# Optimization experiments

Hardware: AMD Instinct MI355X
Metric: run time of the kernel (lower is better)

The kernel has to match this reference:

```python
import jax, jax.numpy as jnp
import numpy as np

DIM = 768
HEADS = 12
HEAD_DIM = DIM // HEADS
B, N = 4, 2048


def setup_inputs() -> dict:
    key = jax.random.key(0)
    ks = jax.random.split(key, 5)
    s = 0.02
    return {
        "x": jax.random.normal(ks[0], (B, N, DIM), dtype=jnp.float32),
        "w_qkv": jax.random.normal(ks[1], (DIM, 3 * DIM), dtype=jnp.float32) * s,
        "b_qkv": jnp.zeros((3 * DIM,), dtype=jnp.float32),
        "w_proj": jax.random.normal(ks[2], (DIM, DIM), dtype=jnp.float32) * s,
        "b_proj": jnp.zeros((DIM,), dtype=jnp.float32),
    }


def reference(x, w_qkv, b_qkv, w_proj, b_proj):
    b, n, c = x.shape
    scale = HEAD_DIM ** -0.5
    qkv = x @ w_qkv + b_qkv                       # [B,N,3C]
    qkv = qkv.reshape(b, n, 3, HEADS, HEAD_DIM)
    q = qkv[:, :, 0].transpose(0, 2, 1, 3)        # [B,H,N,D]
    k = qkv[:, :, 1].transpose(0, 2, 1, 3)
    v = qkv[:, :, 2].transpose(0, 2, 1, 3)
    attn = jnp.einsum("bhqd,bhkd->bhqk", q, k) * scale
    attn = jax.nn.softmax(attn, axis=-1)
    out = jnp.einsum("bhqk,bhkd->bhqd", attn, v)  # [B,H,N,D]
    out = out.transpose(0, 2, 1, 3).reshape(b, n, c)
    return out @ w_proj + b_proj
```

## Files before the change

### kernel.cpp

```cpp
#include <hip/hip_runtime.h>

typedef short sh8 __attribute__((ext_vector_type(8)));
typedef short sh4 __attribute__((ext_vector_type(4)));
typedef float f32x4 __attribute__((ext_vector_type(4)));
typedef float f32x16 __attribute__((ext_vector_type(16)));
typedef unsigned u32x4 __attribute__((ext_vector_type(4)));

extern "C" __device__ float __ocml_native_exp2_f32(float);

__device__ __forceinline__ short f2bf(float f) {
  unsigned u = __builtin_bit_cast(unsigned, f);
  u += 0x7fffu + ((u >> 16) & 1u);
  return (short)(u >> 16);
}

__device__ __forceinline__ void gload16(const short* g, short* l) {
  __builtin_amdgcn_global_load_lds(
      (const __attribute__((address_space(1))) unsigned*)g,
      (__attribute__((address_space(3))) unsigned*)l, 16, 0, 0);
}

__global__ void cast_f32_bf16(const float* __restrict__ in, short* __restrict__ out, int n) {
  int i = (blockIdx.x * blockDim.x + threadIdx.x) * 4;
  if (i >= n) return;
  float4 f = *(const float4*)(in + i);
  sh4 o;
  o.x = f2bf(f.x); o.y = f2bf(f.y); o.z = f2bf(f.z); o.w = f2bf(f.w);
  *(sh4*)(out + i) = o;
}

__global__ void transpose_cast(const float* __restrict__ in, short* __restrict__ out, int K, int Nn) {
  int idx = blockIdx.x * blockDim.x + threadIdx.x;
  if (idx >= K * Nn) return;
  int k = idx / Nn;
  int n = idx - k * Nn;
  out[(size_t)n * K + k] = f2bf(in[idx]);
}

template <int OUTF32>
__global__ __launch_bounds__(256) void gemm_bt(
    const short* __restrict__ A, const short* __restrict__ Bt,
    const float* __restrict__ bias, void* __restrict__ Cv,
    int M, int Nn, int K) {
  __shared__ short As[2][128][32];
  __shared__ short Bs[2][128][32];
  const int t = threadIdx.x;
  const int wave = t >> 6, lane = t & 63, quad = lane >> 4, l15 = lane & 15;
  const int wm = (wave >> 1) * 64, wn = (wave & 1) * 64;
  const int row0 = blockIdx.y * 128, col0 = blockIdx.x * 128;
  f32x4 acc[4][4] = {};

  const int srow = t >> 2;
  const int ssl = ((t & 3) ^ ((t >> 3) & 3)) * 8;
  const short* Asrc0 = A + (size_t)(row0 + srow) * K + ssl;
  const short* Asrc1 = A + (size_t)(row0 + 64 + srow) * K + ssl;
  const short* Bsrc0 = Bt + (size_t)(col0 + srow) * K + ssl;
  const short* Bsrc1 = Bt + (size_t)(col0 + 64 + srow) * K + ssl;
  short* AsF = &As[0][0][0];
  short* BsF = &Bs[0][0][0];
  const int wdst = wave * 512;

  const int soA = (quad ^ ((l15 >> 1) & 3)) * 8;

  gload16(Asrc0, AsF + wdst);
  gload16(Asrc1, AsF + 2048 + wdst);
  gload16(Bsrc0, BsF + wdst);
  gload16(Bsrc1, BsF + 2048 + wdst);
  __syncthreads();

  int cur = 0;
  for (int k0 = 0; k0 < K; k0 += 32) {
    if (k0 + 32 < K) {
      short* Ad = AsF + (cur ^ 1) * 4096 + wdst;
      short* Bd = BsF + (cur ^ 1) * 4096 + wdst;
      gload16(Asrc0 + k0 + 32, Ad);
      gload16(Asrc1 + k0 + 32, Ad + 2048);
      gload16(Bsrc0 + k0 + 32, Bd);
      gload16(Bsrc1 + k0 + 32, Bd + 2048);
    }
    const short* Ab = AsF + cur * 4096;
    const short* Bb = BsF + cur * 4096;
    sh8 af[4], bfv[4];
#pragma unroll
    for (int i = 0; i < 4; i++) af[i] = *(const sh8*)&Ab[(wm + i * 16 + l15) * 32 + soA];
#pragma unroll
    for (int j = 0; j < 4; j++) bfv[j] = *(const sh8*)&Bb[(wn + j * 16 + l15) * 32 + soA];
#pragma unroll
    for (int i = 0; i < 4; i++)
#pragma unroll
      for (int j = 0; j < 4; j++)
        acc[i][j] = __builtin_amdgcn_mfma_f32_16x16x32_bf16(af[i], bfv[j], acc[i][j], 0, 0, 0);
    __syncthreads();
    cur ^= 1;
  }

#pragma unroll
  for (int i = 0; i < 4; i++)
#pragma unroll
    for (int j = 0; j < 4; j++) {
      int r = row0 + wm + i * 16 + quad * 4;
      int c = col0 + wn + j * 16 + l15;
      float bv = bias[c];
#pragma unroll
      for (int e = 0; e < 4; e++) {
        float v = acc[i][j][e] + bv;
        if (OUTF32)
          ((float*)Cv)[(size_t)(r + e) * Nn + c] = v;
        else
          ((short*)Cv)[(size_t)(r + e) * Nn + c] = f2bf(v);
      }
    }
}

__global__ __launch_bounds__(256) void gemm_qkv(
    const short* __restrict__ A, const short* __restrict__ Bt,
    const float* __restrict__ bias,
    short* __restrict__ Qh, short* __restrict__ Kh, short* __restrict__ Vh) {
  const int K = 768;
  __shared__ short As[2][128][32];
  __shared__ short Bs[2][128][32];
  const int t = threadIdx.x;
  const int wave = t >> 6, lane = t & 63, quad = lane >> 4, l15 = lane & 15;
  const int wm = (wave >> 1) * 64, wn = (wave & 1) * 64;
  const int row0 = blockIdx.y * 128, col0 = blockIdx.x * 128;
  f32x4 acc[4][4] = {};

  const int srow = t >> 2;
  const int ssl = ((t & 3) ^ ((t >> 3) & 3)) * 8;
  const short* Asrc0 = A + (size_t)(row0 + srow) * K + ssl;
  const short* Asrc1 = A + (size_t)(row0 + 64 + srow) * K + ssl;
  const short* Bsrc0 = Bt + (size_t)(col0 + srow) * K + ssl;
  const short* Bsrc1 = Bt + (size_t)(col0 + 64 + srow) * K + ssl;
  short* AsF = &As[0][0][0];
  short* BsF = &Bs[0][0][0];
  const int wdst = wave * 512;

  const int soA = (quad ^ ((l15 >> 1) & 3)) * 8;

  gload16(Asrc0, AsF + wdst);
  gload16(Asrc1, AsF + 2048 + wdst);
  gload16(Bsrc0, BsF + wdst);
  gload16(Bsrc1, BsF + 2048 + wdst);
  __syncthreads();

  int cur = 0;
  for (int k0 = 0; k0 < K; k0 += 32) {
    if (k0 + 32 < K) {
      short* Ad = AsF + (cur ^ 1) * 4096 + wdst;
      short* Bd = BsF + (cur ^ 1) * 4096 + wdst;
      gload16(Asrc0 + k0 + 32, Ad);
      gload16(Asrc1 + k0 + 32, Ad + 2048);
      gload16(Bsrc0 + k0 + 32, Bd);
      gload16(Bsrc1 + k0 + 32, Bd + 2048);
    }
    const short* Ab = AsF + cur * 4096;
    const short* Bb = BsF + cur * 4096;
    sh8 af[4], bfv[4];
#pragma unroll
    for (int i = 0; i < 4; i++) af[i] = *(const sh8*)&Ab[(wm + i * 16 + l15) * 32 + soA];
#pragma unroll
    for (int j = 0; j < 4; j++) bfv[j] = *(const sh8*)&Bb[(wn + j * 16 + l15) * 32 + soA];
#pragma unroll
    for (int i = 0; i < 4; i++)
#pragma unroll
      for (int j = 0; j < 4; j++)
        acc[i][j] = __builtin_amdgcn_mfma_f32_16x16x32_bf16(af[i], bfv[j], acc[i][j], 0, 0, 0);
    __syncthreads();
    cur ^= 1;
  }

  const int s = col0 >= 1536 ? 2 : (col0 >= 768 ? 1 : 0);
  short* dst = s == 0 ? Qh : (s == 1 ? Kh : Vh);
  const float scl = (s == 0) ? 0.18033688011112042f : 1.0f;

#pragma unroll
  for (int j = 0; j < 4; j++) {
    int c = col0 + wn + j * 16 + l15;
    int hd = c - s * 768;
    int h = hd >> 6;
    float bv = bias[c];
#pragma unroll
    for (int i = 0; i < 4; i++) {
      int rbase = row0 + wm + i * 16 + quad * 4;
#pragma unroll
      for (int e = 0; e < 4; e++) {
        int r = rbase + e;
        int b = r >> 11, n = r & 2047;
        float v = (acc[i][j][e] + bv) * scl;
        dst[(size_t)(b * 12 + h) * 131072 + n * 64 + (hd & 63)] = f2bf(v);
      }
    }
  }
}

__global__ __launch_bounds__(256) void transpose_v(const short* __restrict__ Vh,
                                                   short* __restrict__ VhT) {
  __shared__ short Tl[64][72];
  const int bid = blockIdx.x;
  const int bh = bid >> 5, nt = bid & 31;
  const size_t hb = (size_t)bh * 131072;
  const int t = threadIdx.x;
  const int r0 = t >> 3;
  const int c0 = (t & 7) * 8;
  sh8 a = *(const sh8*)&Vh[hb + (size_t)(nt * 64 + r0) * 64 + c0];
  sh8 b = *(const sh8*)&Vh[hb + (size_t)(nt * 64 + r0 + 32) * 64 + c0];
#pragma unroll
  for (int j = 0; j < 8; j++) Tl[c0 + j][r0] = a[j];
#pragma unroll
  for (int j = 0; j < 8; j++) Tl[c0 + j][r0 + 32] = b[j];
  __syncthreads();
  uint4 w0 = *(const uint4*)&Tl[r0][c0];
  uint4 w1 = *(const uint4*)&Tl[r0 + 32][c0];
  *(uint4*)&VhT[hb + (size_t)r0 * 2048 + nt * 64 + c0] = w0;
  *(uint4*)&VhT[hb + (size_t)(r0 + 32) * 2048 + nt * 64 + c0] = w1;
}

__global__ __launch_bounds__(256, 3) void attn6(const short* __restrict__ Qh,
                                                const short* __restrict__ Kh,
                                                const short* __restrict__ VhT,
                                                short* __restrict__ outb) {
  const int bid = blockIdx.x;
  const int qb = bid / 48;
  const int bh = bid - qb * 48;
  const int t = threadIdx.x;
  const int w = t >> 6, lane = t & 63;
  const int l31 = lane & 31, hi = lane >> 5;

  __shared__ short Kl[2][64][64];
  __shared__ short Vt[2][64][64];

  const size_t hb = (size_t)bh * 131072;

  sh8 qa[4];
  {
    const short* qp = Qh + hb + (size_t)(qb * 128 + w * 32 + l31) * 64 + hi * 8;
    qa[0] = *(const sh8*)(qp);
    qa[1] = *(const sh8*)(qp + 16);
    qa[2] = *(const sh8*)(qp + 32);
    qa[3] = *(const sh8*)(qp + 48);
  }

  f32x16 o[2] = {};
  f32x4 lsv = {};

  const int srow = t >> 3;
  const int ssl = ((t & 7) ^ (srow & 7)) * 8;
  const short* Ksrc = Kh + hb + (size_t)srow * 64 + ssl;
  const short* Vsrc = VhT + hb + (size_t)srow * 2048 + ssl;
  short* KlF = &Kl[0][0][0];
  short* VtF = &Vt[0][0][0];
  const int wdst = w * 512;

  const int sw7 = l31 & 7;
  int rsl[4];
#pragma unroll
  for (int ks = 0; ks < 4; ks++) rsl[ks] = (((ks << 1) | hi) ^ sw7) * 8;

  gload16(Ksrc, KlF + wdst);
  gload16(Ksrc + (size_t)32 * 64, KlF + 2048 + wdst);
  gload16(Vsrc, VtF + wdst);
  gload16(Vsrc + (size_t)32 * 2048, VtF + 2048 + wdst);
  __syncthreads();

  int cur = 0;
  for (int kt = 0; kt < 32; kt++) {
    if (kt < 31) {
      const int key0 = (kt + 1) * 64;
      short* Kd = KlF + (cur ^ 1) * 4096 + wdst;
      short* Vd = VtF + (cur ^ 1) * 4096 + wdst;
      gload16(Ksrc + (size_t)key0 * 64, Kd);
      gload16(Ksrc + (size_t)(key0 + 32) * 64, Kd + 2048);
      gload16(Vsrc + key0, Vd);
      gload16(Vsrc + (size_t)32 * 2048 + key0, Vd + 2048);
    }

    const short* Kb = KlF + cur * 4096;
    const short* Vb = VtF + cur * 4096;

    sh8 pa[4];
#pragma unroll
    for (int kb = 0; kb < 2; kb++) {
      const short* kr = Kb + (kb * 32 + l31) * 64;
      f32x16 s = {};
#pragma unroll
      for (int ks = 0; ks < 4; ks++)
        s = __builtin_amdgcn_mfma_f32_32x32x16_bf16(*(const sh8*)(kr + rsl[ks]), qa[ks], s, 0, 0, 0);
      unsigned u[8];
#pragma unroll
      for (int m = 0; m < 8; m++) {
        float e0 = __ocml_native_exp2_f32(s[2 * m]);
        float e1 = __ocml_native_exp2_f32(s[2 * m + 1]);
        lsv[m & 3] += e0 + e1;
        asm("v_cvt_pk_bf16_f32 %0, %1, %2" : "=v"(u[m]) : "v"(e0), "v"(e1));
      }
      unsigned y0 = (unsigned)__shfl_xor((int)(hi ? u[0] : u[2]), 32, 64);
      unsigned y1 = (unsigned)__shfl_xor((int)(hi ? u[1] : u[3]), 32, 64);
      unsigned y2 = (unsigned)__shfl_xor((int)(hi ? u[4] : u[6]), 32, 64);
      unsigned y3 = (unsigned)__shfl_xor((int)(hi ? u[5] : u[7]), 32, 64);
      unsigned w0 = hi ? y0 : u[0];
      unsigned w1 = hi ? y1 : u[1];
      unsigned w2 = hi ? u[2] : y0;
      unsigned w3 = hi ? u[3] : y1;
      unsigned w4 = hi ? y2 : u[4];
      unsigned w5 = hi ? y3 : u[5];
      unsigned w6 = hi ? u[6] : y2;
      unsigned w7 = hi ? u[7] : y3;
      u32x4 A0 = {w0, w1, w2, w3};
      u32x4 A1 = {w4, w5, w6, w7};
      pa[2 * kb] = __builtin_bit_cast(sh8, A0);
      pa[2 * kb + 1] = __builtin_bit_cast(sh8, A1);
    }

    __builtin_amdgcn_s_setprio(1);
#pragma unroll
    for (int db = 0; db < 2; db++) {
      const short* vr = Vb + (db * 32 + l31) * 64;
#pragma unroll
      for (int ks = 0; ks < 4; ks++)
        o[db] = __builtin_amdgcn_mfma_f32_32x32x16_bf16(pa[ks], *(const sh8*)(vr + rsl[ks]), o[db], 0, 0, 0);
    }
    __builtin_amdgcn_s_setprio(0);
    __syncthreads();
    cur ^= 1;
  }

  float ls = lsv[0] + lsv[1] + lsv[2] + lsv[3];
  ls += __shfl_xor(ls, 32, 64);
  float inv = 1.f / ls;

  const int b = bh / 12, hh = bh - b * 12;
#pragma unroll
  for (int r = 0; r < 16; r++) {
    int qr = (r & 3) + 8 * (r >> 2) + 4 * hi;
    float iv = __shfl(inv, qr, 64);
    int n = qb * 128 + w * 32 + qr;
    short* op = outb + (size_t)(b * 2048 + n) * 768 + hh * 64 + l31;
    op[0] = f2bf(o[0][r] * iv);
    op[32] = f2bf(o[1][r] * iv);
  }
}

extern "C" void kernel_launch(void* const* d_in, const int* in_sizes, int n_in,
                              void* d_out, int out_size, void* d_ws, size_t ws_size,
                              hipStream_t stream) {
  const float* x = (const float*)d_in[0];
  const float* w_qkv = (const float*)d_in[1];
  const float* b_qkv = (const float*)d_in[2];
  const float* w_proj = (const float*)d_in[3];
  const float* b_proj = (const float*)d_in[4];
  float* out = (float*)d_out;

  char* p = (char*)d_ws;
  short* xb = (short*)p;     p += (size_t)8192 * 768 * 2;
  short* wqkvT = (short*)p;  p += (size_t)2304 * 768 * 2;
  short* wprojT = (short*)p; p += (size_t)768 * 768 * 2;
  short* Qh = (short*)p;     p += (size_t)48 * 131072 * 2;
  short* Kh = (short*)p;     p += (size_t)48 * 131072 * 2;
  short* Vh = (short*)p;     p += (size_t)48 * 131072 * 2;
  short* attnb = (short*)p;  p += (size_t)8192 * 768 * 2;
  short* VhT = xb;

  cast_f32_bf16<<<(8192 * 768 / 4) / 256, 256, 0, stream>>>(x, xb, 8192 * 768);
  transpose_cast<<<(768 * 2304 + 255) / 256, 256, 0, stream>>>(w_qkv, wqkvT, 768, 2304);
  transpose_cast<<<(768 * 768 + 255) / 256, 256, 0, stream>>>(w_proj, wprojT, 768, 768);

  dim3 g1(2304 / 128, 8192 / 128);
  gemm_qkv<<<g1, 256, 0, stream>>>(xb, wqkvT, b_qkv, Qh, Kh, Vh);

  transpose_v<<<48 * 32, 256, 0, stream>>>(Vh, VhT);

  attn6<<<16 * 48, 256, 0, stream>>>(Qh, Kh, VhT, attnb);

  dim3 g2(768 / 128, 8192 / 128);
  gemm_bt<1><<<g2, 256, 0, stream>>>(attnb, wprojT, b_proj, out, 8192, 768, 768);
}
```

Before: 248.8 us.

## Triple-buffer LDS tiles with prefetch distance two and partial vmcnt waits

```diff
diff --git a/kernel.cpp b/kernel.cpp
--- a/kernel.cpp
+++ b/kernel.cpp
@@ -18,6 +18,17 @@
   __builtin_amdgcn_global_load_lds(
       (const __attribute__((address_space(1))) unsigned*)g,
       (__attribute__((address_space(3))) unsigned*)l, 16, 0, 0);
+}
+
+__device__ __forceinline__ void wait4_barrier() {
+  asm volatile("s_waitcnt vmcnt(4)" ::: "memory");
+  __builtin_amdgcn_s_barrier();
+  asm volatile("" ::: "memory");
+}
+__device__ __forceinline__ void wait0_barrier() {
+  asm volatile("s_waitcnt vmcnt(0)" ::: "memory");
+  __builtin_amdgcn_s_barrier();
+  asm volatile("" ::: "memory");
 }
 
 __global__ void cast_f32_bf16(const float* __restrict__ in, short* __restrict__ out, int n) {
@@ -42,8 +53,8 @@
     const short* __restrict__ A, const short* __restrict__ Bt,
     const float* __restrict__ bias, void* __restrict__ Cv,
     int M, int Nn, int K) {
-  __shared__ short As[2][128][32];
-  __shared__ short Bs[2][128][32];
+  __shared__ short As[3][128][32];
+  __shared__ short Bs[3][128][32];
   const int t = threadIdx.x;
   const int wave = t >> 6, lane = t & 63, quad = lane >> 4, l15 = lane & 15;
   const int wm = (wave >> 1) * 64, wn = (wave & 1) * 64;
@@ -62,24 +73,32 @@
 
   const int soA = (quad ^ ((l15 >> 1) & 3)) * 8;
 
-  gload16(Asrc0, AsF + wdst);
-  gload16(Asrc1, AsF + 2048 + wdst);
-  gload16(Bsrc0, BsF + wdst);
-  gload16(Bsrc1, BsF + 2048 + wdst);
-  __syncthreads();
-
-  int cur = 0;
-  for (int k0 = 0; k0 < K; k0 += 32) {
-    if (k0 + 32 < K) {
-      short* Ad = AsF + (cur ^ 1) * 4096 + wdst;
-      short* Bd = BsF + (cur ^ 1) * 4096 + wdst;
-      gload16(Asrc0 + k0 + 32, Ad);
-      gload16(Asrc1 + k0 + 32, Ad + 2048);
-      gload16(Bsrc0 + k0 + 32, Bd);
-      gload16(Bsrc1 + k0 + 32, Bd + 2048);
-    }
-    const short* Ab = AsF + cur * 4096;
-    const short* Bb = BsF + cur * 4096;
+  const int T = K >> 5;
+#pragma unroll
+  for (int pt = 0; pt < 2; pt++) {
+    short* Ad = AsF + pt * 4096 + wdst;
+    short* Bd = BsF + pt * 4096 + wdst;
+    const int k0 = pt * 32;
+    gload16(Asrc0 + k0, Ad);
+    gload16(Asrc1 + k0, Ad + 2048);
+    gload16(Bsrc0 + k0, Bd);
+    gload16(Bsrc1 + k0, Bd + 2048);
+  }
+
+  int rb = 0, wb = 2;
+  for (int tt = 0; tt < T; tt++) {
+    if (tt + 1 < T) wait4_barrier(); else wait0_barrier();
+    if (tt + 2 < T) {
+      const int k0 = (tt + 2) * 32;
+      short* Ad = AsF + wb * 4096 + wdst;
+      short* Bd = BsF + wb * 4096 + wdst;
+      gload16(Asrc0 + k0, Ad);
+      gload16(Asrc1 + k0, Ad + 2048);
+      gload16(Bsrc0 + k0, Bd);
+      gload16(Bsrc1 + k0, Bd + 2048);
+    }
+    const short* Ab = AsF + rb * 4096;
+    const short* Bb = BsF + rb * 4096;
     sh8 af[4], bfv[4];
 #pragma unroll
     for (int i = 0; i < 4; i++) af[i] = *(const sh8*)&Ab[(wm + i * 16 + l15) * 32 + soA];
@@ -90,8 +109,8 @@
 #pragma unroll
       for (int j = 0; j < 4; j++)
         acc[i][j] = __builtin_amdgcn_mfma_f32_16x16x32_bf16(af[i], bfv[j], acc[i][j], 0, 0, 0);
-    __syncthreads();
-    cur ^= 1;
+    rb = rb == 2 ? 0 : rb + 1;
+    wb = wb == 2 ? 0 : wb + 1;
   }
 
 #pragma unroll
@@ -117,8 +136,8 @@
     const float* __restrict__ bias,
     short* __restrict__ Qh, short* __restrict__ Kh, short* __restrict__ Vh) {
   const int K = 768;
-  __shared__ short As[2][128][32];
-  __shared__ short Bs[2][128][32];
+  __shared__ short As[3][128][32];
+  __shared__ short Bs[3][128][32];
   const int t = threadIdx.x;
   const int wave = t >> 6, lane = t & 63, quad = lane >> 4, l15 = lane & 15;
   const int wm = (wave >> 1) * 64, wn = (wave & 1) * 64;
@@ -137,24 +156,32 @@
 
   const int soA = (quad ^ ((l15 >> 1) & 3)) * 8;
 
-  gload16(Asrc0, AsF + wdst);
-  gload16(Asrc1, AsF + 2048 + wdst);
-  gload16(Bsrc0, BsF + wdst);
-  gload16(Bsrc1, BsF + 2048 + wdst);
-  __syncthreads();
-
-  int cur = 0;
-  for (int k0 = 0; k0 < K; k0 += 32) {
-    if (k0 + 32 < K) {
-      short* Ad = AsF + (cur ^ 1) * 4096 + wdst;
-      short* Bd = BsF + (cur ^ 1) * 4096 + wdst;
-      gload16(Asrc0 + k0 + 32, Ad);
-      gload16(Asrc1 + k0 + 32, Ad + 2048);
-      gload16(Bsrc0 + k0 + 32, Bd);
-      gload16(Bsrc1 + k0 + 32, Bd + 2048);
-    }
-    const short* Ab = AsF + cur * 4096;
-    const short* Bb = BsF + cur * 4096;
+  const int T = K >> 5;
+#pragma unroll
+  for (int pt = 0; pt < 2; pt++) {
+    short* Ad = AsF + pt * 4096 + wdst;
+    short* Bd = BsF + pt * 4096 + wdst;
+    const int k0 = pt * 32;
+    gload16(Asrc0 + k0, Ad);
+    gload16(Asrc1 + k0, Ad + 2048);
+    gload16(Bsrc0 + k0, Bd);
+    gload16(Bsrc1 + k0, Bd + 2048);
+  }
+
+  int rb = 0, wb = 2;
+  for (int tt = 0; tt < T; tt++) {
+    if (tt + 1 < T) wait4_barrier(); else wait0_barrier();
+    if (tt + 2 < T) {
+      const int k0 = (tt + 2) * 32;
+      short* Ad = AsF + wb * 4096 + wdst;
+      short* Bd = BsF + wb * 4096 + wdst;
+      gload16(Asrc0 + k0, Ad);
+      gload16(Asrc1 + k0, Ad + 2048);
+      gload16(Bsrc0 + k0, Bd);
+      gload16(Bsrc1 + k0, Bd + 2048);
+    }
+    const short* Ab = AsF + rb * 4096;
+    const short* Bb = BsF + rb * 4096;
     sh8 af[4], bfv[4];
 #pragma unroll
     for (int i = 0; i < 4; i++) af[i] = *(const sh8*)&Ab[(wm + i * 16 + l15) * 32 + soA];
@@ -165,8 +192,8 @@
 #pragma unroll
       for (int j = 0; j < 4; j++)
         acc[i][j] = __builtin_amdgcn_mfma_f32_16x16x32_bf16(af[i], bfv[j], acc[i][j], 0, 0, 0);
-    __syncthreads();
-    cur ^= 1;
+    rb = rb == 2 ? 0 : rb + 1;
+    wb = wb == 2 ? 0 : wb + 1;
   }
 
   const int s = col0 >= 1536 ? 2 : (col0 >= 768 ? 1 : 0);
@@ -215,7 +242,7 @@
   *(uint4*)&VhT[hb + (size_t)(r0 + 32) * 2048 + nt * 64 + c0] = w1;
 }
 
-__global__ __launch_bounds__(256, 3) void attn6(const short* __restrict__ Qh,
+__global__ __launch_bounds__(256, 3) void attn7(const short* __restrict__ Qh,
                                                 const short* __restrict__ Kh,
                                                 const short* __restrict__ VhT,
                                                 short* __restrict__ outb) {
@@ -226,8 +253,8 @@
   const int w = t >> 6, lane = t & 63;
   const int l31 = lane & 31, hi = lane >> 5;
 
-  __shared__ short Kl[2][64][64];
-  __shared__ short Vt[2][64][64];
+  __shared__ short Kl[3][64][64];
+  __shared__ short Vt[3][64][64];
 
   const size_t hb = (size_t)bh * 131072;
 
@@ -239,6 +266,7 @@
     qa[2] = *(const sh8*)(qp + 32);
     qa[3] = *(const sh8*)(qp + 48);
   }
+  asm volatile("s_waitcnt vmcnt(0)" ::: "memory");
 
   f32x16 o[2] = {};
   f32x4 lsv = {};
@@ -256,26 +284,32 @@
 #pragma unroll
   for (int ks = 0; ks < 4; ks++) rsl[ks] = (((ks << 1) | hi) ^ sw7) * 8;
 
-  gload16(Ksrc, KlF + wdst);
-  gload16(Ksrc + (size_t)32 * 64, KlF + 2048 + wdst);
-  gload16(Vsrc, VtF + wdst);
-  gload16(Vsrc + (size_t)32 * 2048, VtF + 2048 + wdst);
-  __syncthreads();
-
-  int cur = 0;
+#pragma unroll
+  for (int pt = 0; pt < 2; pt++) {
+    const int key0 = pt * 64;
+    short* Kd = KlF + pt * 4096 + wdst;
+    short* Vd = VtF + pt * 4096 + wdst;
+    gload16(Ksrc + (size_t)key0 * 64, Kd);
+    gload16(Ksrc + (size_t)(key0 + 32) * 64, Kd + 2048);
+    gload16(Vsrc + key0, Vd);
+    gload16(Vsrc + (size_t)32 * 2048 + key0, Vd + 2048);
+  }
+
+  int rb = 0, wb = 2;
   for (int kt = 0; kt < 32; kt++) {
-    if (kt < 31) {
-      const int key0 = (kt + 1) * 64;
-      short* Kd = KlF + (cur ^ 1) * 4096 + wdst;
-      short* Vd = VtF + (cur ^ 1) * 4096 + wdst;
+    if (kt < 31) wait4_barrier(); else wait0_barrier();
+    if (kt < 30) {
+      const int key0 = (kt + 2) * 64;
+      short* Kd = KlF + wb * 4096 + wdst;
+      short* Vd = VtF + wb * 4096 + wdst;
       gload16(Ksrc + (size_t)key0 * 64, Kd);
       gload16(Ksrc + (size_t)(key0 + 32) * 64, Kd + 2048);
       gload16(Vsrc + key0, Vd);
       gload16(Vsrc + (size_t)32 * 2048 + key0, Vd + 2048);
     }
 
-    const short* Kb = KlF + cur * 4096;
-    const short* Vb = VtF + cur * 4096;
+    const short* Kb = KlF + rb * 4096;
+    const short* Vb = VtF + rb * 4096;
 
     sh8 pa[4];
 #pragma unroll
@@ -320,8 +354,8 @@
         o[db] = __builtin_amdgcn_mfma_f32_32x32x16_bf16(pa[ks], *(const sh8*)(vr + rsl[ks]), o[db], 0, 0, 0);
     }
     __builtin_amdgcn_s_setprio(0);
-    __syncthreads();
-    cur ^= 1;
+    rb = rb == 2 ? 0 : rb + 1;
+    wb = wb == 2 ? 0 : wb + 1;
   }
 
   float ls = lsv[0] + lsv[1] + lsv[2] + lsv[3];
@@ -369,7 +403,7 @@
 
   transpose_v<<<48 * 32, 256, 0, stream>>>(Vh, VhT);
 
-  attn6<<<16 * 48, 256, 0, stream>>>(Qh, Kh, VhT, attnb);
+  attn7<<<16 * 48, 256, 0, stream>>>(Qh, Kh, VhT, attnb);
 
   dim3 g2(768 / 128, 8192 / 128);
   gemm_bt<1><<<g2, 256, 0, stream>>>(attnb, wprojT, b_proj, out, 8192, 768, 768);
```

Result: no change. 245.0 us (-1.5%).
